# Performance work log

Hardware: AMD Instinct MI355X
Metric: run time of the kernel (lower is better)

## Reference

```python
import jax, jax.numpy as jnp
import numpy as np

N_TOKENS = 131072
HIDDEN = 1024       # hp.HIDDEN_SIZE
CLUSTER = 64        # hp.TOPIC_CLUSTER_SIZE
EXPERTS = 64        # hp.NUMBER_OF_EXPERTS
EPS = 1e-8


def _l2_normalize(x, eps=EPS):
    # F.normalize: x / max(||x||_2, eps) along last dim
    n = jnp.linalg.norm(x, axis=-1, keepdims=True)
    return x / jnp.maximum(n, eps)


def setup_inputs() -> dict:
    key = jax.random.key(0)
    k1, k2, k3, k4 = jax.random.split(key, 4)
    x = jax.random.normal(k1, (N_TOKENS, HIDDEN), dtype=jnp.float32)
    # nn.Linear(HIDDEN, CLUSTER) weight/bias
    W = jax.random.normal(k2, (HIDDEN, CLUSTER), dtype=jnp.float32) * 0.02
    b = jax.random.normal(k3, (CLUSTER,), dtype=jnp.float32) * 0.02
    # torch.rand -> uniform [0,1)
    centroids = jax.random.uniform(k4, (EXPERTS, CLUSTER), dtype=jnp.float32)
    return {"last_hidden_states": x, "W": W, "b": b, "centroids": centroids, "k": 2}


def reference(last_hidden_states, W, b, centroids, k):
    # distillation: Linear + exact GELU
    h = jax.nn.gelu(last_hidden_states @ W + b, approximate=False)  # [N, C]
    d = _l2_normalize(h)                                            # [N, C]
    c = _l2_normalize(centroids)                                    # [E, C]
    # torch.cdist (p=2): sqrt(|a|^2 + |b|^2 - 2 a.b), clamped at 0
    sq = (jnp.sum(d * d, axis=-1, keepdims=True)
          + jnp.sum(c * c, axis=-1)[None, :]
          - 2.0 * (d @ c.T))                                        # [N, E]
    distances = jnp.sqrt(jnp.maximum(sq, 0.0))
    probabilities = jax.nn.softmax(-distances, axis=-1)             # [N, E]
    top_k_probabilities, top_k_indices = jax.lax.top_k(probabilities, k)
    return top_k_probabilities, top_k_indices
```

## Files before the change

kernel.cpp:

```cpp
#include <hip/hip_runtime.h>
#include <math.h>

#define N_TOK   131072
#define HID     1024
#define CL      64
#define NEXP    64
#define KC      32
#define NC      (HID / KC)
#define TPW     16
#define TPB     64
#define TAU     3e-5f

#define WS_CNT   0
#define WS_LIST  16
#define WS_CN    (16 + N_TOK * 4)
#define WS_CN2   (WS_CN + NEXP * CL * 4)
#define WS_CND   (WS_CN2 + NEXP * 4)
#define WS_CN2D  (WS_CND + NEXP * CL * 8)

__device__ __forceinline__ float wave_sum(float v) {
#pragma unroll
    for (int off = 32; off > 0; off >>= 1) v += __shfl_xor(v, off, 64);
    return v;
}
__device__ __forceinline__ double wave_sum_d(double v) {
#pragma unroll
    for (int off = 32; off > 0; off >>= 1) v += __shfl_xor(v, off, 64);
    return v;
}
__device__ __forceinline__ double wave_max_d(double v) {
#pragma unroll
    for (int off = 32; off > 0; off >>= 1) v = fmax(v, __shfl_xor(v, off, 64));
    return v;
}
__device__ __forceinline__ void wave_argmax(float& v, int& idx) {
#pragma unroll
    for (int off = 32; off > 0; off >>= 1) {
        float v2 = __shfl_xor(v, off, 64);
        int   i2 = __shfl_xor(idx, off, 64);
        if (v2 > v || (v2 == v && i2 < idx)) { v = v2; idx = i2; }
    }
}
__device__ __forceinline__ void wave_argmax_d(double& v, int& idx) {
#pragma unroll
    for (int off = 32; off > 0; off >>= 1) {
        double v2 = __shfl_xor(v, off, 64);
        int    i2 = __shfl_xor(idx, off, 64);
        if (v2 > v || (v2 == v && i2 < idx)) { v = v2; idx = i2; }
    }
}

#define GLL16(gp, lp) __builtin_amdgcn_global_load_lds(                       \
    (const __attribute__((address_space(1))) void*)(gp),                      \
    (__attribute__((address_space(3))) void*)(lp), 16, 0, 0)

extern "C" __global__ void prep_centroids(const float* __restrict__ cent,
                                          float* __restrict__ cn,
                                          float* __restrict__ cn2,
                                          double* __restrict__ cnd,
                                          double* __restrict__ cn2d,
                                          int* __restrict__ cnt) {
    int e = threadIdx.x;
    if (e == 0) *cnt = 0;
    double s = 0.0;
#pragma unroll
    for (int j = 0; j < CL; j++) { double v = (double)cent[e * CL + j]; s += v * v; }
    double nrm = fmax(sqrt(s), 1e-8);
    double s2 = 0.0;
#pragma unroll
    for (int j = 0; j < CL; j++) {
        double c = (double)cent[e * CL + j] / nrm;
        cnd[e * CL + j] = c;
        cn[e * CL + j] = (float)c;
        s2 += c * c;
    }
    cn2d[e] = s2;
    cn2[e] = (float)s2;
}

extern "C" __global__ void __launch_bounds__(256, 4)
router_main(const float* __restrict__ x, const float* __restrict__ W,
            const float* __restrict__ bias, const float* __restrict__ cn,
            const float* __restrict__ cn2, float* __restrict__ out,
            int* __restrict__ cnt, int* __restrict__ list) {
    __shared__ float sX[2][TPB][KC];
    __shared__ float sW[2][KC][CL];

    const int tid  = threadIdx.x;
    const int lane = tid & 63;
    const int wv   = __builtin_amdgcn_readfirstlane(tid >> 6);
    const int tok0 = blockIdx.x * TPB;
    const int twave = tok0 + wv * TPW;

    const size_t xoff0 = (size_t)(twave + 0 + (lane >> 3)) * HID + (size_t)((lane & 7) * 4);
    const size_t xoff1 = (size_t)(twave + 8 + (lane >> 3)) * HID + (size_t)((lane & 7) * 4);
    const int woffb = wv * 512 + lane * 4;

#define STAGE(buf, kc) do {                                                   \
        GLL16(x + xoff0 + (kc), &sX[buf][wv * TPW + 0][0]);                   \
        GLL16(x + xoff1 + (kc), &sX[buf][wv * TPW + 8][0]);                   \
        GLL16(W + (size_t)(kc) * CL + woffb,                                  \
              (char*)&sW[buf][0][0] + (wv * 2 + 0) * 1024);                   \
        GLL16(W + (size_t)(kc) * CL + woffb + 256,                            \
              (char*)&sW[buf][0][0] + (wv * 2 + 1) * 1024);                   \
    } while (0)

    float acc[TPW];
#pragma unroll
    for (int i = 0; i < TPW; i++) acc[i] = 0.f;

    STAGE(0, 0);
    for (int c = 0; c < NC; ++c) {
        __syncthreads();
        if (c + 1 < NC) STAGE((c + 1) & 1, (c + 1) * KC);
        const int cur = c & 1;
        for (int k = 0; k < KC; k += 4) {
            const float w0 = sW[cur][k + 0][lane];
            const float w1 = sW[cur][k + 1][lane];
            const float w2 = sW[cur][k + 2][lane];
            const float w3 = sW[cur][k + 3][lane];
#pragma unroll
            for (int i = 0; i < TPW; i++) {
                const float4 xv = *(const float4*)&sX[cur][wv * TPW + i][k];
                acc[i] = fmaf(xv.x, w0, acc[i]);
                acc[i] = fmaf(xv.y, w1, acc[i]);
                acc[i] = fmaf(xv.z, w2, acc[i]);
                acc[i] = fmaf(xv.w, w3, acc[i]);
            }
        }
    }
    __syncthreads();

    float (*sD)[CL] = (float (*)[CL]) & sX[0][0][0];

    const float bj = bias[lane];
    const float myCn2 = cn2[lane];
    float d2[TPW];
#pragma unroll
    for (int i = 0; i < TPW; i++) {
        float h = acc[i] + bj;
        float g = 0.5f * h * (1.f + erff(h * 0.70710678118654752440f));
        float n2 = wave_sum(g * g);
        float nrm = fmaxf(sqrtf(n2), 1e-8f);
        float d = g / nrm;
        d2[i] = wave_sum(d * d);
        sD[wv * TPW + i][lane] = d;
    }

    float dot[TPW];
#pragma unroll
    for (int i = 0; i < TPW; i++) dot[i] = 0.f;
    const float* crow = cn + (size_t)lane * CL;
    for (int j = 0; j < CL; j += 4) {
        const float4 c4 = *(const float4*)(crow + j);
#pragma unroll
        for (int i = 0; i < TPW; i++) {
            const float4 d4 = *(const float4*)&sD[wv * TPW + i][j];
            dot[i] = fmaf(d4.x, c4.x, fmaf(d4.y, c4.y,
                     fmaf(d4.z, c4.z, fmaf(d4.w, c4.w, dot[i]))));
        }
    }

#pragma unroll 1
    for (int i = 0; i < TPW; i++) {
        float sq   = d2[i] + myCn2 - 2.f * dot[i];
        float dist = sqrtf(fmaxf(sq, 0.f));
        float nd   = -dist;

        float a1 = nd; int j1 = lane; wave_argmax(a1, j1);
        float nd2m = (lane == j1) ? -1e30f : nd;
        float a2 = nd2m; int j2 = lane; wave_argmax(a2, j2);
        float nd3m = (lane == j2) ? -1e30f : nd2m;
        float a3 = nd3m; int j3 = lane; wave_argmax(a3, j3);

        float e    = expf(nd - a1);
        float ssum = wave_sum(e);
        float p    = e / ssum;
        float p1   = __shfl(p, j1, 64);
        float p2   = __shfl(p, j2, 64);

        bool flag = ((a1 - a2) < TAU) || ((a2 - a3) < TAU);

        if (lane == 0) {
            size_t t = (size_t)(twave + i);
            out[t * 2 + 0] = p1;
            out[t * 2 + 1] = p2;
            out[(size_t)N_TOK * 2 + t * 2 + 0] = (float)j1;
            out[(size_t)N_TOK * 2 + t * 2 + 1] = (float)j2;
            if (flag) { int ix = atomicAdd(cnt, 1); list[ix] = (int)t; }
        }
    }
#undef STAGE
}

extern "C" __global__ void __launch_bounds__(64)
router_rescue(const float* __restrict__ x, const float* __restrict__ W,
              const float* __restrict__ bias, const double* __restrict__ cnd,
              const double* __restrict__ cn2d, const int* __restrict__ list,
              const int* __restrict__ cnt, float* __restrict__ out) {
    __shared__ float  sx[HID];
    __shared__ double sd[CL];
    const int lane = threadIdx.x;
    const int n = *cnt;

    for (int fi = blockIdx.x; fi < n; fi += gridDim.x) {
        __syncthreads();
        const int t = list[fi];
        for (int k = lane; k < HID; k += 64) sx[k] = x[(size_t)t * HID + k];
        __syncthreads();

        double h0 = 0.0, h1 = 0.0, h2 = 0.0, h3 = 0.0;
        const float* Wp = W + lane;
        for (int k = 0; k < HID; k += 4) {
            h0 += (double)sx[k + 0] * (double)Wp[(k + 0) * CL];
            h1 += (double)sx[k + 1] * (double)Wp[(k + 1) * CL];
            h2 += (double)sx[k + 2] * (double)Wp[(k + 2) * CL];
            h3 += (double)sx[k + 3] * (double)Wp[(k + 3) * CL];
        }
        double h = (h0 + h1) + (h2 + h3) + (double)bias[lane];
        double g = 0.5 * h * (1.0 + erf(h * 0.70710678118654752440));
        double n2 = wave_sum_d(g * g);
        double nrm = fmax(sqrt(n2), 1e-8);
        double d = g / nrm;
        double d2 = wave_sum_d(d * d);
        sd[lane] = d;
        __syncthreads();

        double dot = 0.0;
        const double* ce = cnd + (size_t)lane * CL;
#pragma unroll 8
        for (int j = 0; j < CL; j++) dot += sd[j] * ce[j];

        double sq   = d2 + cn2d[lane] - 2.0 * dot;
        double dist = sqrt(fmax(sq, 0.0));
        double nd   = -dist;
        double m    = wave_max_d(nd);
        double e    = exp(nd - m);
        double ssum = wave_sum_d(e);
        double p    = e / ssum;

        double a1 = nd; int j1 = lane; wave_argmax_d(a1, j1);
        double ndm = (lane == j1) ? -1e300 : nd;
        double a2 = ndm; int j2 = lane; wave_argmax_d(a2, j2);
        double p1 = __shfl(p, j1, 64);
        double p2 = __shfl(p, j2, 64);

        if (lane == 0) {
            out[(size_t)t * 2 + 0] = (float)p1;
            out[(size_t)t * 2 + 1] = (float)p2;
            out[(size_t)N_TOK * 2 + (size_t)t * 2 + 0] = (float)j1;
            out[(size_t)N_TOK * 2 + (size_t)t * 2 + 1] = (float)j2;
        }
    }
}

extern "C" void kernel_launch(void* const* d_in, const int* in_sizes, int n_in,
                              void* d_out, int out_size, void* d_ws, size_t ws_size,
                              hipStream_t stream) {
    const float* x    = (const float*)d_in[0];
    const float* W    = (const float*)d_in[1];
    const float* bias = (const float*)d_in[2];
    const float* cent = (const float*)d_in[3];

    char* wsb = (char*)d_ws;
    int*    cnt  = (int*)(wsb + WS_CNT);
    int*    list = (int*)(wsb + WS_LIST);
    float*  cn   = (float*)(wsb + WS_CN);
    float*  cn2  = (float*)(wsb + WS_CN2);
    double* cnd  = (double*)(wsb + WS_CND);
    double* cn2d = (double*)(wsb + WS_CN2D);
    float*  out  = (float*)d_out;

    prep_centroids<<<1, 64, 0, stream>>>(cent, cn, cn2, cnd, cn2d, cnt);
    router_main<<<N_TOK / TPB, 256, 0, stream>>>(x, W, bias, cn, cn2, out, cnt, list);
    router_rescue<<<4096, 64, 0, stream>>>(x, W, bias, cnd, cn2d, list, cnt, out);
}
```

Measured before the change: 1.248 ms.

## Register-tile the projection GEMM 8x8 per thread with 256-token blocks

Each thread now computes an 8-token by 8-channel register tile instead of one channel for 16 tokens, and each block handles 256 tokens (64 per wave) rather than 64. This cuts LDS reads per FMA by reusing loaded x and W values across the tile. The GELU/normalize stage uses 8-lane shuffle reductions, and the distance stage keeps centroid rows in registers while looping over 64 tokens per wave. In exchange, register pressure rises and occupancy is lowered to 2 blocks per SM via the launch bounds.

After: 1.130 ms. -9.5%, faster.

```diff
diff --git a/kernel.cpp b/kernel.cpp
--- a/kernel.cpp
+++ b/kernel.cpp
@@ -7,8 +7,7 @@
 #define NEXP    64
 #define KC      32
 #define NC      (HID / KC)
-#define TPW     16
-#define TPB     64
+#define TPB     256
 #define TAU     3e-5f
 
 #define WS_CNT   0
@@ -78,7 +77,7 @@
     cn2[e] = (float)s2;
 }
 
-extern "C" __global__ void __launch_bounds__(256, 4)
+extern "C" __global__ void __launch_bounds__(256, 2)
 router_main(const float* __restrict__ x, const float* __restrict__ W,
             const float* __restrict__ bias, const float* __restrict__ cn,
             const float* __restrict__ cn2, float* __restrict__ out,
@@ -89,81 +88,145 @@
     const int tid  = threadIdx.x;
     const int lane = tid & 63;
     const int wv   = __builtin_amdgcn_readfirstlane(tid >> 6);
+    const int tg   = lane >> 3;
+    const int dg   = lane & 7;
     const int tok0 = blockIdx.x * TPB;
-    const int twave = tok0 + wv * TPW;
-
-    const size_t xoff0 = (size_t)(twave + 0 + (lane >> 3)) * HID + (size_t)((lane & 7) * 4);
-    const size_t xoff1 = (size_t)(twave + 8 + (lane >> 3)) * HID + (size_t)((lane & 7) * 4);
-    const int woffb = wv * 512 + lane * 4;
+
+    const size_t xoff = (size_t)(tok0 + wv * 64 + (lane >> 3)) * HID + (size_t)((lane & 7) * 4);
+    const int woff = (wv * 8 + (lane >> 4)) * CL + (lane & 15) * 4;
 
 #define STAGE(buf, kc) do {                                                   \
-        GLL16(x + xoff0 + (kc), &sX[buf][wv * TPW + 0][0]);                   \
-        GLL16(x + xoff1 + (kc), &sX[buf][wv * TPW + 8][0]);                   \
-        GLL16(W + (size_t)(kc) * CL + woffb,                                  \
-              (char*)&sW[buf][0][0] + (wv * 2 + 0) * 1024);                   \
-        GLL16(W + (size_t)(kc) * CL + woffb + 256,                            \
-              (char*)&sW[buf][0][0] + (wv * 2 + 1) * 1024);                   \
+        _Pragma("unroll")                                                     \
+        for (int q = 0; q < 8; ++q)                                           \
+            GLL16(x + xoff + (size_t)q * 8 * HID + (kc),                      \
+                  &sX[buf][wv * 64 + q * 8][0]);                              \
+        GLL16(W + (size_t)(kc) * CL + woff,       &sW[buf][wv * 8][0]);       \
+        GLL16(W + (size_t)(kc) * CL + woff + 256, &sW[buf][wv * 8 + 4][0]);   \
     } while (0)
 
-    float acc[TPW];
-#pragma unroll
-    for (int i = 0; i < TPW; i++) acc[i] = 0.f;
+    float acc[8][8];
+#pragma unroll
+    for (int t = 0; t < 8; ++t)
+#pragma unroll
+        for (int d = 0; d < 8; ++d) acc[t][d] = 0.f;
 
     STAGE(0, 0);
+#pragma unroll 1
     for (int c = 0; c < NC; ++c) {
         __syncthreads();
         if (c + 1 < NC) STAGE((c + 1) & 1, (c + 1) * KC);
         const int cur = c & 1;
-        for (int k = 0; k < KC; k += 4) {
-            const float w0 = sW[cur][k + 0][lane];
-            const float w1 = sW[cur][k + 1][lane];
-            const float w2 = sW[cur][k + 2][lane];
-            const float w3 = sW[cur][k + 3][lane];
-#pragma unroll
-            for (int i = 0; i < TPW; i++) {
-                const float4 xv = *(const float4*)&sX[cur][wv * TPW + i][k];
-                acc[i] = fmaf(xv.x, w0, acc[i]);
-                acc[i] = fmaf(xv.y, w1, acc[i]);
-                acc[i] = fmaf(xv.z, w2, acc[i]);
-                acc[i] = fmaf(xv.w, w3, acc[i]);
+        const float* xb = &sX[cur][wv * 64 + tg * 8][0];
+        const float* wb = &sW[cur][0][dg * 8];
+#pragma unroll
+        for (int k4 = 0; k4 < KC / 4; ++k4) {
+            float4 xq[8];
+#pragma unroll
+            for (int tt = 0; tt < 8; ++tt)
+                xq[tt] = *(const float4*)(xb + tt * KC + k4 * 4);
+#pragma unroll
+            for (int kk = 0; kk < 4; ++kk) {
+                const float4 wA = *(const float4*)(wb + (k4 * 4 + kk) * CL);
+                const float4 wB = *(const float4*)(wb + (k4 * 4 + kk) * CL + 4);
+#pragma unroll
+                for (int tt = 0; tt < 8; ++tt) {
+                    const float xv = (kk == 0) ? xq[tt].x : (kk == 1) ? xq[tt].y
+                                   : (kk == 2) ? xq[tt].z : xq[tt].w;
+                    acc[tt][0] = fmaf(xv, wA.x, acc[tt][0]);
+                    acc[tt][1] = fmaf(xv, wA.y, acc[tt][1]);
+                    acc[tt][2] = fmaf(xv, wA.z, acc[tt][2]);
+                    acc[tt][3] = fmaf(xv, wA.w, acc[tt][3]);
+                    acc[tt][4] = fmaf(xv, wB.x, acc[tt][4]);
+                    acc[tt][5] = fmaf(xv, wB.y, acc[tt][5]);
+                    acc[tt][6] = fmaf(xv, wB.z, acc[tt][6]);
+                    acc[tt][7] = fmaf(xv, wB.w, acc[tt][7]);
+                }
             }
         }
     }
     __syncthreads();
 
-    float (*sD)[CL] = (float (*)[CL]) & sX[0][0][0];
-
-    const float bj = bias[lane];
+    const int d0   = dg * 8;
+    const int trow = wv * 64 + tg * 8;
+
+    const float4 b0 = *(const float4*)(bias + d0);
+    const float4 b1 = *(const float4*)(bias + d0 + 4);
+    const float bq[8] = {b0.x, b0.y, b0.z, b0.w, b1.x, b1.y, b1.z, b1.w};
+
+    float g[8][8];
+    float n2[8];
+#pragma unroll
+    for (int tt = 0; tt < 8; ++tt) {
+        float s = 0.f;
+#pragma unroll
+        for (int dd = 0; dd < 8; ++dd) {
+            float h = acc[tt][dd] + bq[dd];
+            float gv = 0.5f * h * (1.f + erff(h * 0.70710678118654752440f));
+            g[tt][dd] = gv;
+            s = fmaf(gv, gv, s);
+        }
+        n2[tt] = s;
+    }
+#pragma unroll
+    for (int tt = 0; tt < 8; ++tt) {
+        n2[tt] += __shfl_xor(n2[tt], 1, 64);
+        n2[tt] += __shfl_xor(n2[tt], 2, 64);
+        n2[tt] += __shfl_xor(n2[tt], 4, 64);
+    }
+
+    float (*sD)[CL] = (float (*)[CL])&sX[0][0][0];
+    float* sN = (float*)&sW[0][0][0];
+
+    float d2[8];
+#pragma unroll
+    for (int tt = 0; tt < 8; ++tt) {
+        float nrm = fmaxf(sqrtf(n2[tt]), 1e-8f);
+        float inv = 1.f / nrm;
+        float4 w0, w1;
+        w0.x = g[tt][0] * inv; w0.y = g[tt][1] * inv;
+        w0.z = g[tt][2] * inv; w0.w = g[tt][3] * inv;
+        w1.x = g[tt][4] * inv; w1.y = g[tt][5] * inv;
+        w1.z = g[tt][6] * inv; w1.w = g[tt][7] * inv;
+        float s2 = 0.f;
+        s2 = fmaf(w0.x, w0.x, s2); s2 = fmaf(w0.y, w0.y, s2);
+        s2 = fmaf(w0.z, w0.z, s2); s2 = fmaf(w0.w, w0.w, s2);
+        s2 = fmaf(w1.x, w1.x, s2); s2 = fmaf(w1.y, w1.y, s2);
+        s2 = fmaf(w1.z, w1.z, s2); s2 = fmaf(w1.w, w1.w, s2);
+        *(float4*)&sD[trow + tt][d0]     = w0;
+        *(float4*)&sD[trow + tt][d0 + 4] = w1;
+        d2[tt] = s2;
+    }
+#pragma unroll
+    for (int tt = 0; tt < 8; ++tt) {
+        d2[tt] += __shfl_xor(d2[tt], 1, 64);
+        d2[tt] += __shfl_xor(d2[tt], 2, 64);
+        d2[tt] += __shfl_xor(d2[tt], 4, 64);
+    }
+    if (dg == 0) {
+#pragma unroll
+        for (int tt = 0; tt < 8; ++tt) sN[trow + tt] = d2[tt];
+    }
+
+    float4 cq[16];
+#pragma unroll
+    for (int j = 0; j < 16; ++j)
+        cq[j] = *(const float4*)(cn + (size_t)lane * CL + j * 4);
     const float myCn2 = cn2[lane];
-    float d2[TPW];
-#pragma unroll
-    for (int i = 0; i < TPW; i++) {
-        float h = acc[i] + bj;
-        float g = 0.5f * h * (1.f + erff(h * 0.70710678118654752440f));
-        float n2 = wave_sum(g * g);
-        float nrm = fmaxf(sqrtf(n2), 1e-8f);
-        float d = g / nrm;
-        d2[i] = wave_sum(d * d);
-        sD[wv * TPW + i][lane] = d;
-    }
-
-    float dot[TPW];
-#pragma unroll
-    for (int i = 0; i < TPW; i++) dot[i] = 0.f;
-    const float* crow = cn + (size_t)lane * CL;
-    for (int j = 0; j < CL; j += 4) {
-        const float4 c4 = *(const float4*)(crow + j);
-#pragma unroll
-        for (int i = 0; i < TPW; i++) {
-            const float4 d4 = *(const float4*)&sD[wv * TPW + i][j];
-            dot[i] = fmaf(d4.x, c4.x, fmaf(d4.y, c4.y,
-                     fmaf(d4.z, c4.z, fmaf(d4.w, c4.w, dot[i]))));
-        }
-    }
+    const float* drow = &sD[wv * 64][0];
 
 #pragma unroll 1
-    for (int i = 0; i < TPW; i++) {
-        float sq   = d2[i] + myCn2 - 2.f * dot[i];
+    for (int tl = 0; tl < 64; ++tl) {
+        const float* dp = drow + tl * CL;
+        float dot = 0.f;
+#pragma unroll
+        for (int j = 0; j < 16; ++j) {
+            const float4 dv = *(const float4*)(dp + j * 4);
+            dot = fmaf(dv.x, cq[j].x, fmaf(dv.y, cq[j].y,
+                  fmaf(dv.z, cq[j].z, fmaf(dv.w, cq[j].w, dot))));
+        }
+        const float d2b = sN[wv * 64 + tl];
+
+        float sq   = d2b + myCn2 - 2.f * dot;
         float dist = sqrtf(fmaxf(sq, 0.f));
         float nd   = -dist;
 
@@ -182,7 +245,7 @@
         bool flag = ((a1 - a2) < TAU) || ((a2 - a3) < TAU);
 
         if (lane == 0) {
-            size_t t = (size_t)(twave + i);
+            size_t t = (size_t)(tok0 + wv * 64 + tl);
             out[t * 2 + 0] = p1;
             out[t * 2 + 1] = p2;
             out[(size_t)N_TOK * 2 + t * 2 + 0] = (float)j1;
```
